# Kernel tuning notes

Measured on AMD Instinct MI355X. Metric: run time of the kernel, lower is better.

Reference implementation:

```python
import jax, jax.numpy as jnp
import numpy as np

N_NODES = 50000
N_EDGES = 800000
IN_DIM = 128
HID = 32
HEADS = 4


def _lin_init(key, fan_in, fan_out):
    k1, k2 = jax.random.split(key)
    s = 1.0 / np.sqrt(fan_in)
    W = jax.random.uniform(k1, (fan_in, fan_out), jnp.float32, -s, s)
    b = jax.random.uniform(k2, (fan_out,), jnp.float32, -s, s)
    return W, b


def setup_inputs() -> dict:
    key = jax.random.key(0)
    keys = jax.random.split(key, 12)
    x = jax.random.normal(keys[0], (N_NODES, IN_DIM), jnp.float32)
    edge_index = jax.random.randint(keys[1], (2, N_EDGES), 0, N_NODES, jnp.int64)

    # conv1: in_dim -> heads*hid (128 -> 4*32)
    Wq1, bq1 = _lin_init(keys[2], IN_DIM, HEADS * HID)
    Wk1, bk1 = _lin_init(keys[3], IN_DIM, HEADS * HID)
    Wv1, bv1 = _lin_init(keys[4], IN_DIM, HEADS * HID)
    Ws1, bs1 = _lin_init(keys[5], IN_DIM, HEADS * HID)
    # conv2: 128 -> 1*32
    Wq2, bq2 = _lin_init(keys[6], HEADS * HID, HID)
    Wk2, bk2 = _lin_init(keys[7], HEADS * HID, HID)
    Wv2, bv2 = _lin_init(keys[8], HEADS * HID, HID)
    Ws2, bs2 = _lin_init(keys[9], HEADS * HID, HID)
    # output linear: 32 -> 1
    Wo, bo = _lin_init(keys[10], HID, 1)

    return {
        "x": x, "edge_index": edge_index,
        "Wq1": Wq1, "bq1": bq1, "Wk1": Wk1, "bk1": bk1,
        "Wv1": Wv1, "bv1": bv1, "Ws1": Ws1, "bs1": bs1,
        "Wq2": Wq2, "bq2": bq2, "Wk2": Wk2, "bk2": bk2,
        "Wv2": Wv2, "bv2": bv2, "Ws2": Ws2, "bs2": bs2,
        "Wo": Wo, "bo": bo,
    }


def transformer_conv(x, edge_index, Wq, bq, Wk, bk, Wv, bv, Ws, bs, heads, d):
    # PyG TransformerConv (concat=True, root_weight=True, beta=False, no edge attr).
    n = x.shape[0]
    src, dst = edge_index[0], edge_index[1]  # message j(src) -> i(dst)
    q = (x @ Wq + bq).reshape(n, heads, d)
    k = (x @ Wk + bk).reshape(n, heads, d)
    v = (x @ Wv + bv).reshape(n, heads, d)
    # per-edge attention logits [E, heads]
    logits = (q[dst] * k[src]).sum(-1) / jnp.sqrt(jnp.float32(d))
    # segment softmax over incoming edges of each target node
    m = jax.ops.segment_max(logits, dst, num_segments=n)
    p = jnp.exp(logits - m[dst])
    denom = jax.ops.segment_sum(p, dst, num_segments=n)
    alpha = p / denom[dst]  # [E, heads]
    # weighted scatter-add of values
    msg = alpha[:, :, None] * v[src]  # [E, heads, d]
    aggr = jax.ops.segment_sum(msg, dst, num_segments=n).reshape(n, heads * d)
    return aggr + x @ Ws + bs  # root (skip) connection


def reference(x, edge_index,
              Wq1, bq1, Wk1, bk1, Wv1, bv1, Ws1, bs1,
              Wq2, bq2, Wk2, bk2, Wv2, bv2, Ws2, bs2,
              Wo, bo):
    h = transformer_conv(x, edge_index, Wq1, bq1, Wk1, bk1, Wv1, bv1, Ws1, bs1, HEADS, HID)
    h = jax.nn.relu(h)
    h = transformer_conv(h, edge_index, Wq2, bq2, Wk2, bk2, Wv2, bv2, Ws2, bs2, 1, HID)
    h = jax.nn.relu(h)
    g = h.mean(axis=0)  # [HID]
    return g @ Wo + bo  # [1]
```

## Files before the change

kernel.cpp:

```cpp
#include <hip/hip_runtime.h>
#include <math.h>

#define N_NODES 50000
#define N_EDGES 800000
#define NBK 196
#define BCAP 6144

typedef short short8 __attribute__((ext_vector_type(8)));
typedef float f32x4 __attribute__((ext_vector_type(4)));
typedef float f32x2 __attribute__((ext_vector_type(2)));

__device__ inline unsigned short f2bf(float v) {
  unsigned u = __float_as_uint(v);
  u += 0x7FFFu + ((u >> 16) & 1u);
  return (unsigned short)(u >> 16);
}
__device__ inline float bf2f(unsigned short b) {
  return __uint_as_float(((unsigned)b) << 16);
}
__device__ inline float bflo(unsigned u) { return __uint_as_float(u << 16); }
__device__ inline float bfhi(unsigned u) { return __uint_as_float(u & 0xFFFF0000u); }
__device__ inline unsigned char f2fp8(float v) {
  return (unsigned char)(__builtin_amdgcn_cvt_pk_fp8_f32(v, 0.f, 0, false) & 0xFF);
}
template <bool HI>
__device__ inline f32x2 fp8dec(unsigned u) {
  return __builtin_amdgcn_cvt_pk_f32_fp8(u, HI);
}

#define SCL 0.17677669529663687f

#define W1_B 256
#define W2_B 64
__global__ void prep_fused(const float* __restrict__ Wq1, const float* __restrict__ Wk1,
                           const float* __restrict__ Wv1, const float* __restrict__ Ws1,
                           const float* __restrict__ bq1, const float* __restrict__ bk1,
                           const float* __restrict__ bv1, const float* __restrict__ bs1,
                           const float* __restrict__ Wq2, const float* __restrict__ Wk2,
                           const float* __restrict__ Wv2, const float* __restrict__ Ws2,
                           const float* __restrict__ bq2, const float* __restrict__ bk2,
                           const float* __restrict__ bv2, const float* __restrict__ bs2,
                           unsigned short* __restrict__ Wt1, float* __restrict__ bcat1,
                           unsigned short* __restrict__ Wt2, float* __restrict__ bcat2,
                           const int* __restrict__ ei, int* __restrict__ bhist, int E) {
  const int b = blockIdx.x, tid = threadIdx.x;
  if (b < W1_B) {
    int i = b * 256 + tid;
    int c = i >> 7, k = i & 127;
    int mi = c >> 7, lc = c & 127;
    const float* W = (mi == 0) ? Wq1 : (mi == 1) ? Wk1 : (mi == 2) ? Wv1 : Ws1;
    float scl = (mi == 0) ? SCL : 1.f;
    Wt1[i] = f2bf(W[(size_t)k * 128 + lc] * scl);
    if (i < 512) {
      int bm = i >> 7, bl = i & 127;
      const float* bb = (bm == 0) ? bq1 : (bm == 1) ? bk1 : (bm == 2) ? bv1 : bs1;
      bcat1[i] = bb[bl] * ((bm == 0) ? SCL : 1.f);
    }
  } else if (b < W1_B + W2_B) {
    int i = (b - W1_B) * 256 + tid;
    int c = i >> 7, k = i & 127;
    int mi = c >> 5, lc = c & 31;
    const float* W = (mi == 0) ? Wq2 : (mi == 1) ? Wk2 : (mi == 2) ? Wv2 : Ws2;
    float scl = (mi == 0) ? SCL : 1.f;
    Wt2[i] = f2bf(W[(size_t)k * 32 + lc] * scl);
    if (i < 128) {
      int bm = i >> 5, bl = i & 31;
      const float* bb = (bm == 0) ? bq2 : (bm == 1) ? bk2 : (bm == 2) ? bv2 : bs2;
      bcat2[i] = bb[bl] * ((bm == 0) ? SCL : 1.f);
    }
  } else {
    __shared__ int h[NBK];
    for (int i = tid; i < NBK; i += 256) h[i] = 0;
    __syncthreads();
    int e = (b - W1_B - W2_B) * 4096 + tid;
#pragma unroll
    for (int p = 0; p < 16; ++p, e += 256)
      if (e < E) atomicAdd(&h[ei[E + e] >> 8], 1);
    __syncthreads();
    for (int i = tid; i < NBK; i += 256)
      if (h[i]) atomicAdd(&bhist[i], h[i]);
  }
}

__global__ void bucket_scan(const int* __restrict__ bhist, int* __restrict__ boff,
                            int* __restrict__ bcur) {
  __shared__ int s[256];
  int t = threadIdx.x;
  int v = (t < NBK) ? bhist[t] : 0;
  s[t] = v;
  __syncthreads();
#pragma unroll
  for (int off = 1; off < 256; off <<= 1) {
    int u = (t >= off) ? s[t - off] : 0;
    __syncthreads();
    s[t] += u;
    __syncthreads();
  }
  if (t < NBK) {
    int excl = s[t] - v;
    boff[t] = excl;
    bcur[t] = excl;
  }
  if (t == NBK - 1) boff[NBK] = s[t];
}

__global__ __launch_bounds__(256) void scatter_gemm1(
    const int* __restrict__ ei, int* __restrict__ bcur, int* __restrict__ ebuck, int E, int EB,
    const float* __restrict__ X, const unsigned short* __restrict__ Wt,
    const float* __restrict__ bcat, unsigned short* __restrict__ Q1b,
    unsigned short* __restrict__ SK1, unsigned char* __restrict__ KV8, int M) {
  __shared__ __align__(16) unsigned char L[3][64 * 272];
  const int tid = threadIdx.x;

  if ((int)blockIdx.x < EB) {
    int* lh = (int*)L[0];
    for (int i = tid; i < NBK; i += 256) lh[i] = 0;
    __syncthreads();
    const int e0 = blockIdx.x * 4096;
    int pks[16], bks[16];
#pragma unroll
    for (int p = 0; p < 16; ++p) {
      int e = e0 + p * 256 + tid;
      if (e < E) {
        int src = ei[e], dst = ei[E + e];
        pks[p] = (src << 8) | (dst & 255);
        bks[p] = dst >> 8;
        atomicAdd(&lh[bks[p]], 1);
      } else bks[p] = -1;
    }
    __syncthreads();
    for (int i = tid; i < NBK; i += 256)
      if (lh[i]) lh[i] = atomicAdd(&bcur[i], lh[i]);
    __syncthreads();
#pragma unroll
    for (int p = 0; p < 16; ++p) {
      if (bks[p] >= 0) {
        int slot = atomicAdd(&lh[bks[p]], 1);
        ebuck[slot] = pks[p];
      }
    }
    return;
  }

  unsigned short* As = (unsigned short*)L[0];
  const int bm = (blockIdx.x - EB) * 64;
  const int wave = tid >> 6, lane = tid & 63;
  const int lr = lane & 15, q = lane >> 4;

#pragma unroll
  for (int p = 0; p < 8; ++p) {
    int f = tid + p * 256;
    int row = f >> 5, c4 = f & 31;
    int gm = bm + row; if (gm >= M) gm = 0;
    float4 v = *(const float4*)(X + (size_t)gm * 128 + c4 * 4);
    ushort4 o;
    o.x = f2bf(v.x); o.y = f2bf(v.y); o.z = f2bf(v.z); o.w = f2bf(v.w);
    *(ushort4*)&As[row * 136 + c4 * 4] = o;
  }
  __syncthreads();

  const int colbase = wave * 128;
  f32x4 acc[4][8];
#pragma unroll
  for (int i = 0; i < 4; ++i)
#pragma unroll
    for (int j = 0; j < 8; ++j) acc[i][j] = (f32x4){0.f, 0.f, 0.f, 0.f};

#pragma unroll
  for (int ks = 0; ks < 4; ++ks) {
    short8 af[4];
#pragma unroll
    for (int i = 0; i < 4; ++i)
      af[i] = *(short8*)&As[(i * 16 + lr) * 136 + ks * 32 + q * 8];
#pragma unroll
    for (int j = 0; j < 8; ++j) {
      short8 bf = *(const short8*)(Wt + (size_t)(colbase + j * 16 + lr) * 128 + ks * 32 + q * 8);
#pragma unroll
      for (int i = 0; i < 4; ++i)
        acc[i][j] = __builtin_amdgcn_mfma_f32_16x16x32_bf16(af[i], bf, acc[i][j], 0, 0, 0);
    }
  }
  __syncthreads();

  float bj[8];
#pragma unroll
  for (int j = 0; j < 8; ++j) bj[j] = bcat[colbase + j * 16 + lr];

  if (wave == 0 || wave == 3) {
    unsigned short* Ls16 = (unsigned short*)((wave == 0) ? L[1] : L[0]);
#pragma unroll
    for (int i = 0; i < 4; ++i)
#pragma unroll
      for (int r = 0; r < 4; ++r) {
        int row = i * 16 + q * 4 + r;
#pragma unroll
        for (int j = 0; j < 8; ++j)
          Ls16[row * 136 + j * 16 + lr] = f2bf(acc[i][j][r] + bj[j]);
      }
  } else {
    unsigned char* KLs = L[2];
    const int voff = (wave == 2) ? 2 : 0;
#pragma unroll
    for (int i = 0; i < 4; ++i)
#pragma unroll
      for (int r = 0; r < 4; ++r) {
        int row = i * 16 + q * 4 + r;
#pragma unroll
        for (int j = 0; j < 8; ++j) {
          int d = j * 16 + lr;
          KLs[row * 272 + 4 * (d >> 1) + voff + (d & 1)] = f2fp8(acc[i][j][r] + bj[j]);
        }
      }
  }
  __syncthreads();

#pragma unroll
  for (int p = 0; p < 4; ++p) {
    int f = tid + p * 256;
    int row = f >> 4, u = f & 15;
    int gr = bm + row;
    if (gr < M) {
      *(uint4*)(Q1b + (size_t)gr * 128 + u * 8) = *(uint4*)&((unsigned short*)L[1])[row * 136 + u * 8];
      *(uint4*)(KV8 + (size_t)gr * 256 + u * 16) = *(uint4*)&L[2][row * 272 + u * 16];
      *(uint4*)(SK1 + (size_t)gr * 128 + u * 8) = *(uint4*)&((unsigned short*)L[0])[row * 136 + u * 8];
    }
  }
}

__global__ void bucket_csr(const int* __restrict__ ebuck, const int* __restrict__ boff,
                           int* __restrict__ rowptr, int* __restrict__ esrc, int N) {
  const int b = blockIdx.x;
  const int lo = boff[b], hi = boff[b + 1];
  const int cnt = hi - lo;
  __shared__ int hist[256];
  __shared__ int cur[256];
  __shared__ int sorted[BCAP];
  const int t = threadIdx.x;
  hist[t] = 0;
  __syncthreads();
  for (int i = t; i < cnt; i += 256) atomicAdd(&hist[ebuck[lo + i] & 255], 1);
  __syncthreads();
  int v = hist[t];
  sorted[t] = v;
  __syncthreads();
#pragma unroll
  for (int off = 1; off < 256; off <<= 1) {
    int u = (t >= off) ? sorted[t - off] : 0;
    __syncthreads();
    sorted[t] += u;
    __syncthreads();
  }
  int excl = sorted[t] - v;
  cur[t] = excl;
  int node = b * 256 + t;
  if (node <= N) rowptr[node] = lo + excl;
  __syncthreads();
  for (int i = t; i < cnt; i += 256) {
    int pk = ebuck[lo + i];
    int slot = atomicAdd(&cur[pk & 255], 1);
    if (slot < BCAP) sorted[slot] = pk;
    else esrc[lo + slot] = pk & 0xFFFFFF00;
  }
  __syncthreads();
  int lim = cnt < BCAP ? cnt : BCAP;
  for (int i = t; i < lim; i += 256) esrc[lo + i] = sorted[i] & 0xFFFFFF00;
}

__global__ __launch_bounds__(256) void gemm2(
    const unsigned short* __restrict__ Ab, const unsigned short* __restrict__ Wt,
    const float* __restrict__ bcat, unsigned char* __restrict__ C2b, int M) {
  __shared__ __align__(16) unsigned short As[64 * 136];
  __shared__ __align__(16) unsigned char Lsb[64 * 272];
  const int bm = blockIdx.x * 64;
  const int tid = threadIdx.x, wave = tid >> 6, lane = tid & 63;
  const int lr = lane & 15, q = lane >> 4;

#pragma unroll
  for (int p = 0; p < 4; ++p) {
    int f = tid + p * 256;
    int row = f >> 4, chunk = f & 15;
    int gm = bm + row; if (gm >= M) gm = 0;
    uint4 v = *(const uint4*)(Ab + (size_t)gm * 128 + chunk * 8);
    *(uint4*)&As[row * 136 + chunk * 8] = v;
  }
  __syncthreads();

  f32x4 acc[4][2];
#pragma unroll
  for (int i = 0; i < 4; ++i)
#pragma unroll
    for (int j = 0; j < 2; ++j) acc[i][j] = (f32x4){0.f, 0.f, 0.f, 0.f};

#pragma unroll
  for (int ks = 0; ks < 4; ++ks) {
    short8 af[4];
#pragma unroll
    for (int i = 0; i < 4; ++i)
      af[i] = *(short8*)&As[(i * 16 + lr) * 136 + ks * 32 + q * 8];
#pragma unroll
    for (int j = 0; j < 2; ++j) {
      short8 bf = *(const short8*)(Wt + (size_t)(wave * 32 + j * 16 + lr) * 128 + ks * 32 + q * 8);
#pragma unroll
      for (int i = 0; i < 4; ++i)
        acc[i][j] = __builtin_amdgcn_mfma_f32_16x16x32_bf16(af[i], bf, acc[i][j], 0, 0, 0);
    }
  }

  float bj[2];
#pragma unroll
  for (int j = 0; j < 2; ++j) bj[j] = bcat[wave * 32 + j * 16 + lr];
#pragma unroll
  for (int i = 0; i < 4; ++i)
#pragma unroll
    for (int r = 0; r < 4; ++r) {
      int row = i * 16 + q * 4 + r;
#pragma unroll
      for (int j = 0; j < 2; ++j) {
        int c = wave * 32 + j * 16 + lr;
        float val = acc[i][j][r] + bj[j];
        if (c < 32) {
          *(unsigned short*)&Lsb[row * 272 + 2 * c] = f2bf(val);
        } else if (c < 64) {
          int d = c - 32;
          Lsb[row * 272 + 64 + 4 * (d >> 1) + (d & 1)] = f2fp8(val);
        } else if (c < 96) {
          int d = c - 64;
          Lsb[row * 272 + 64 + 4 * (d >> 1) + 2 + (d & 1)] = f2fp8(val);
        } else {
          *(unsigned short*)&Lsb[row * 272 + 192 + 2 * (c - 96)] = f2bf(val);
        }
      }
    }
  __syncthreads();
#pragma unroll
  for (int p = 0; p < 16; ++p) {
    int idx = tid + p * 256;
    int row = idx >> 6, u = idx & 63;
    int gr = bm + row;
    if (gr < M) *(unsigned*)(C2b + (size_t)gr * 256 + u * 4) = *(const unsigned*)&Lsb[row * 272 + u * 4];
  }
}

__global__ void node_attn1(const int* __restrict__ rowptr, const int* __restrict__ esrc,
                           const unsigned short* __restrict__ Qb,
                           const unsigned char* __restrict__ KV8,
                           const unsigned short* __restrict__ SK, unsigned short* __restrict__ Hb,
                           int n) {
  int node = (blockIdx.x * blockDim.x + threadIdx.x) >> 6;
  int lane = threadIdx.x & 63;
  if (node >= n) return;
  const int half = lane >> 5, ll = lane & 31;
  const int r0 = rowptr[node], r1 = rowptr[node + 1];
  uint2 qq = *(const uint2*)(Qb + (size_t)node * 128 + ll * 4);
  const float q0 = bflo(qq.x), q1 = bfhi(qq.x), q2 = bflo(qq.y), q3 = bfhi(qq.y);
  float l = 0.f, a0 = 0.f, a1 = 0.f, a2 = 0.f, a3 = 0.f;
  const unsigned char* kvb = KV8 + ll * 8;
  int j = r0;
  for (; j + 8 <= r1; j += 8) {
    int e = j + half * 4;
    int s0 = esrc[e], s1 = esrc[e + 1], s2 = esrc[e + 2], s3 = esrc[e + 3];
    uint2 u0 = *(const uint2*)(kvb + s0);
    uint2 u1 = *(const uint2*)(kvb + s1);
    uint2 u2 = *(const uint2*)(kvb + s2);
    uint2 u3 = *(const uint2*)(kvb + s3);
    f32x2 k0a = fp8dec<false>(u0.x), k0b = fp8dec<false>(u0.y);
    f32x2 k1a = fp8dec<false>(u1.x), k1b = fp8dec<false>(u1.y);
    f32x2 k2a = fp8dec<false>(u2.x), k2b = fp8dec<false>(u2.y);
    f32x2 k3a = fp8dec<false>(u3.x), k3b = fp8dec<false>(u3.y);
    float d0 = q0 * k0a.x + q1 * k0a.y + q2 * k0b.x + q3 * k0b.y;
    float d1 = q0 * k1a.x + q1 * k1a.y + q2 * k1b.x + q3 * k1b.y;
    float d2 = q0 * k2a.x + q1 * k2a.y + q2 * k2b.x + q3 * k2b.y;
    float d3 = q0 * k3a.x + q1 * k3a.y + q2 * k3b.x + q3 * k3b.y;
#pragma unroll
    for (int msk = 1; msk <= 4; msk <<= 1) {
      d0 += __shfl_xor(d0, msk);
      d1 += __shfl_xor(d1, msk);
      d2 += __shfl_xor(d2, msk);
      d3 += __shfl_xor(d3, msk);
    }
    float p0 = __expf(d0), p1 = __expf(d1), p2 = __expf(d2), p3 = __expf(d3);
    l += (p0 + p1) + (p2 + p3);
    f32x2 v0a = fp8dec<true>(u0.x), v0b = fp8dec<true>(u0.y);
    f32x2 v1a = fp8dec<true>(u1.x), v1b = fp8dec<true>(u1.y);
    f32x2 v2a = fp8dec<true>(u2.x), v2b = fp8dec<true>(u2.y);
    f32x2 v3a = fp8dec<true>(u3.x), v3b = fp8dec<true>(u3.y);
    a0 += p0 * v0a.x + p1 * v1a.x + p2 * v2a.x + p3 * v3a.x;
    a1 += p0 * v0a.y + p1 * v1a.y + p2 * v2a.y + p3 * v3a.y;
    a2 += p0 * v0b.x + p1 * v1b.x + p2 * v2b.x + p3 * v3b.x;
    a3 += p0 * v0b.y + p1 * v1b.y + p2 * v2b.y + p3 * v3b.y;
  }
  for (; j < r1; j += 4) {
    int eA = j + half * 2, eB = eA + 1;
    bool vA = eA < r1, vB = eB < r1;
    int sA = esrc[vA ? eA : r0];
    int sB = esrc[vB ? eB : r0];
    uint2 ua = *(const uint2*)(kvb + sA);
    uint2 ub = *(const uint2*)(kvb + sB);
    f32x2 ka1 = fp8dec<false>(ua.x), ka2 = fp8dec<false>(ua.y);
    f32x2 kb1 = fp8dec<false>(ub.x), kb2 = fp8dec<false>(ub.y);
    float dA = q0 * ka1.x + q1 * ka1.y + q2 * ka2.x + q3 * ka2.y;
    float dB = q0 * kb1.x + q1 * kb1.y + q2 * kb2.x + q3 * kb2.y;
#pragma unroll
    for (int msk = 1; msk <= 4; msk <<= 1) {
      dA += __shfl_xor(dA, msk);
      dB += __shfl_xor(dB, msk);
    }
    float pA = vA ? __expf(dA) : 0.f;
    float pB = vB ? __expf(dB) : 0.f;
    l += pA + pB;
    f32x2 va1 = fp8dec<true>(ua.x), va2 = fp8dec<true>(ua.y);
    f32x2 vb1 = fp8dec<true>(ub.x), vb2 = fp8dec<true>(ub.y);
    a0 += pA * va1.x + pB * vb1.x;
    a1 += pA * va1.y + pB * vb1.y;
    a2 += pA * va2.x + pB * vb2.x;
    a3 += pA * va2.y + pB * vb2.y;
  }
  l  += __shfl_xor(l, 32);
  a0 += __shfl_xor(a0, 32);
  a1 += __shfl_xor(a1, 32);
  a2 += __shfl_xor(a2, 32);
  a3 += __shfl_xor(a3, 32);
  float inv = (l > 0.f) ? 1.f / l : 0.f;
  if (half == 0) {
    uint2 sk = *(const uint2*)(SK + (size_t)node * 128 + ll * 4);
    float o0 = fmaxf(bflo(sk.x) + a0 * inv, 0.f);
    float o1 = fmaxf(bfhi(sk.x) + a1 * inv, 0.f);
    float o2 = fmaxf(bflo(sk.y) + a2 * inv, 0.f);
    float o3 = fmaxf(bfhi(sk.y) + a3 * inv, 0.f);
    uint2 hb;
    hb.x = ((unsigned)f2bf(o1) << 16) | (unsigned)f2bf(o0);
    hb.y = ((unsigned)f2bf(o3) << 16) | (unsigned)f2bf(o2);
    *(uint2*)(Hb + (size_t)node * 128 + ll * 4) = hb;
  }
}

__global__ void node_attn2(const int* __restrict__ rowptr, const int* __restrict__ esrc,
                           const unsigned char* __restrict__ C2b, const float* __restrict__ Wo,
                           float* __restrict__ pblock, int n) {
  __shared__ float ps[4];
  int node = (blockIdx.x * blockDim.x + threadIdx.x) >> 6;
  int lane = threadIdx.x & 63;
  int wave = threadIdx.x >> 6;
  const int g = lane >> 4, gl = lane & 15;
  float t = 0.f;
  if (node < n) {
    const int r0 = rowptr[node], r1 = rowptr[node + 1];
    unsigned qu = *(const unsigned*)(C2b + (size_t)node * 256 + gl * 4);
    const float q0 = bflo(qu), q1 = bfhi(qu);
    float l = 0.f, a0 = 0.f, a1 = 0.f;
    const unsigned char* kvb = C2b + 64 + gl * 4;
    int j = r0;
    for (; j + 8 <= r1; j += 8) {
      int e = j + g * 2;
      int s0 = esrc[e], s1 = esrc[e + 1];
      unsigned u0 = *(const unsigned*)(kvb + s0);
      unsigned u1 = *(const unsigned*)(kvb + s1);
      f32x2 k0 = fp8dec<false>(u0), k1 = fp8dec<false>(u1);
      float d0 = q0 * k0.x + q1 * k0.y;
      float d1 = q0 * k1.x + q1 * k1.y;
#pragma unroll
      for (int msk = 1; msk <= 8; msk <<= 1) {
        d0 += __shfl_xor(d0, msk);
        d1 += __shfl_xor(d1, msk);
      }
      float p0 = __expf(d0), p1 = __expf(d1);
      l += p0 + p1;
      f32x2 v0 = fp8dec<true>(u0), v1 = fp8dec<true>(u1);
      a0 += p0 * v0.x + p1 * v1.x;
      a1 += p0 * v0.y + p1 * v1.y;
    }
    for (; j < r1; j += 4) {
      bool v = (j + g) < r1;
      int s = esrc[v ? j + g : r0];
      unsigned u = *(const unsigned*)(kvb + s);
      f32x2 kd = fp8dec<false>(u);
      float d = q0 * kd.x + q1 * kd.y;
#pragma unroll
      for (int msk = 1; msk <= 8; msk <<= 1) d += __shfl_xor(d, msk);
      float p = v ? __expf(d) : 0.f;
      l += p;
      f32x2 vd = fp8dec<true>(u);
      a0 += p * vd.x;
      a1 += p * vd.y;
    }
#pragma unroll
    for (int msk = 16; msk <= 32; msk <<= 1) {
      l  += __shfl_xor(l, msk);
      a0 += __shfl_xor(a0, msk);
      a1 += __shfl_xor(a1, msk);
    }
    float inv = (l > 0.f) ? 1.f / l : 0.f;
    unsigned hu = *(const unsigned*)(C2b + (size_t)node * 256 + 192 + gl * 4);
    float o0 = fmaxf(bflo(hu) + a0 * inv, 0.f);
    float o1 = fmaxf(bfhi(hu) + a1 * inv, 0.f);
    t = o0 * Wo[2 * gl] + o1 * Wo[2 * gl + 1];
#pragma unroll
    for (int msk = 1; msk <= 8; msk <<= 1) t += __shfl_xor(t, msk);
  }
  if (lane == 0) ps[wave] = t;
  __syncthreads();
  if (threadIdx.x == 0) pblock[blockIdx.x] = ps[0] + ps[1] + ps[2] + ps[3];
}

__global__ void final_out(const float* __restrict__ pblock, const float* __restrict__ bo,
                          float* __restrict__ out, int nb, float invN) {
  __shared__ float s[256];
  float acc = 0.f;
  for (int i = threadIdx.x; i < nb; i += 256) acc += pblock[i];
  s[threadIdx.x] = acc;
  __syncthreads();
  for (int off = 128; off >= 1; off >>= 1) {
    if (threadIdx.x < off) s[threadIdx.x] += s[threadIdx.x + off];
    __syncthreads();
  }
  if (threadIdx.x == 0) out[0] = s[0] * invN + bo[0];
}

extern "C" void kernel_launch(void* const* d_in, const int* in_sizes, int n_in,
                              void* d_out, int out_size, void* d_ws, size_t ws_size,
                              hipStream_t stream) {
  const float* x   = (const float*)d_in[0];
  const int*   ei  = (const int*)d_in[1];
  const float* Wq1 = (const float*)d_in[2];  const float* bq1 = (const float*)d_in[3];
  const float* Wk1 = (const float*)d_in[4];  const float* bk1 = (const float*)d_in[5];
  const float* Wv1 = (const float*)d_in[6];  const float* bv1 = (const float*)d_in[7];
  const float* Ws1 = (const float*)d_in[8];  const float* bs1 = (const float*)d_in[9];
  const float* Wq2 = (const float*)d_in[10]; const float* bq2 = (const float*)d_in[11];
  const float* Wk2 = (const float*)d_in[12]; const float* bk2 = (const float*)d_in[13];
  const float* Wv2 = (const float*)d_in[14]; const float* bv2 = (const float*)d_in[15];
  const float* Ws2 = (const float*)d_in[16]; const float* bs2 = (const float*)d_in[17];
  const float* Wo  = (const float*)d_in[18]; const float* bo  = (const float*)d_in[19];

  char* ws = (char*)d_ws;
  const int N = N_NODES, E = N_EDGES;
  const int GB = (N + 63) / 64;
  const int EB = (E + 4095) / 4096;
  const int AB = (N * 64) / 256;

  unsigned short* Q1b = (unsigned short*)(ws + 0);
  unsigned short* SK1 = (unsigned short*)(ws + 12800000);
  unsigned char*  KV1 = (unsigned char*)(ws + 25600000);
  unsigned short* H1b = (unsigned short*)(ws + 51200000);
  unsigned char*  C2  = (unsigned char*)(ws + 64000000);
  int* rowptr = (int*)(ws + 89600000);
  int* esrc   = (int*)(ws + 89900032);
  int* bhist  = (int*)(ws + 93100032);
  int* boff   = (int*)(ws + 93101056);
  int* bcur   = (int*)(ws + 93102080);
  unsigned short* Wt1   = (unsigned short*)(ws + 93103104);
  unsigned short* Wt2   = (unsigned short*)(ws + 93234176);
  float*          bcat1 = (float*)(ws + 93266944);
  float*          bcat2 = (float*)(ws + 93268992);
  float*          pblock = (float*)(ws + 93269504);
  int*            ebuck = (int*)(ws + 93319552);

  float* out = (float*)d_out;

  dim3 blk(256);

  hipMemsetAsync(bhist, 0, NBK * sizeof(int), stream);

  prep_fused<<<dim3(W1_B + W2_B + EB), blk, 0, stream>>>(
      Wq1, Wk1, Wv1, Ws1, bq1, bk1, bv1, bs1,
      Wq2, Wk2, Wv2, Ws2, bq2, bk2, bv2, bs2,
      Wt1, bcat1, Wt2, bcat2, ei, bhist, E);

  bucket_scan<<<dim3(1), blk, 0, stream>>>(bhist, boff, bcur);

  scatter_gemm1<<<dim3(EB + GB), blk, 0, stream>>>(
      ei, bcur, ebuck, E, EB, x, Wt1, bcat1, Q1b, SK1, KV1, N);

  bucket_csr<<<dim3(NBK), blk, 0, stream>>>(ebuck, boff, rowptr, esrc, N);

  node_attn1<<<dim3(AB), blk, 0, stream>>>(rowptr, esrc, Q1b, KV1, SK1, H1b, N);

  gemm2<<<dim3(GB), blk, 0, stream>>>(H1b, Wt2, bcat2, C2, N);

  node_attn2<<<dim3(AB), blk, 0, stream>>>(rowptr, esrc, C2, Wo, pblock, N);

  final_out<<<dim3(1), blk, 0, stream>>>(pblock, bo, out, AB, 1.0f / (float)N);
}
```

Before: 253.3 us.

## Build CSR via per-node degree counting and direct atomic scatter

Replaces the two-level bucket sort with a direct build: prep counts per-node in-degree with global atomics, a new multi-block scan produces rowptr and per-node cursors, and the scatter writes each edge's source straight into its CSR slot via a per-node atomic. This drops the bucket_csr kernel and the intermediate ebuck buffer. It also splits the GEMM1 accumulator into two passes with fewer registers and adds launch_bounds occupancy 4. The trade-off is 800k contended global atomics on per-node counters instead of LDS atomics, plus an extra kernel launch.

After: 290.5 us. 14.7% more time.

```diff
diff --git a/kernel.cpp b/kernel.cpp
--- a/kernel.cpp
+++ b/kernel.cpp
@@ -4,7 +4,6 @@
 #define N_NODES 50000
 #define N_EDGES 800000
 #define NBK 196
-#define BCAP 6144
 
 typedef short short8 __attribute__((ext_vector_type(8)));
 typedef float f32x4 __attribute__((ext_vector_type(4)));
@@ -42,7 +41,8 @@
                            const float* __restrict__ bv2, const float* __restrict__ bs2,
                            unsigned short* __restrict__ Wt1, float* __restrict__ bcat1,
                            unsigned short* __restrict__ Wt2, float* __restrict__ bcat2,
-                           const int* __restrict__ ei, int* __restrict__ bhist, int E) {
+                           const int* __restrict__ ei, int* __restrict__ bhist,
+                           int* __restrict__ deg, int E) {
   const int b = blockIdx.x, tid = threadIdx.x;
   if (b < W1_B) {
     int i = b * 256 + tid;
@@ -75,15 +75,18 @@
     int e = (b - W1_B - W2_B) * 4096 + tid;
 #pragma unroll
     for (int p = 0; p < 16; ++p, e += 256)
-      if (e < E) atomicAdd(&h[ei[E + e] >> 8], 1);
+      if (e < E) {
+        int d = ei[E + e];
+        atomicAdd(&h[d >> 8], 1);
+        atomicAdd(&deg[d], 1);
+      }
     __syncthreads();
     for (int i = tid; i < NBK; i += 256)
       if (h[i]) atomicAdd(&bhist[i], h[i]);
   }
 }
 
-__global__ void bucket_scan(const int* __restrict__ bhist, int* __restrict__ boff,
-                            int* __restrict__ bcur) {
+__global__ void bucket_scan(const int* __restrict__ bhist, int* __restrict__ boff) {
   __shared__ int s[256];
   int t = threadIdx.x;
   int v = (t < NBK) ? bhist[t] : 0;
@@ -96,16 +99,32 @@
     s[t] += u;
     __syncthreads();
   }
-  if (t < NBK) {
-    int excl = s[t] - v;
-    boff[t] = excl;
-    bcur[t] = excl;
-  }
+  if (t < NBK) boff[t] = s[t] - v;
   if (t == NBK - 1) boff[NBK] = s[t];
 }
 
-__global__ __launch_bounds__(256) void scatter_gemm1(
-    const int* __restrict__ ei, int* __restrict__ bcur, int* __restrict__ ebuck, int E, int EB,
+__global__ void rowptr_scan(const int* __restrict__ deg, const int* __restrict__ boff,
+                            int* __restrict__ rowptr, int* __restrict__ nodecur) {
+  __shared__ int s[256];
+  const int b = blockIdx.x, t = threadIdx.x;
+  const int node = b * 256 + t;
+  int v = (node < N_NODES) ? deg[node] : 0;
+  s[t] = v;
+  __syncthreads();
+#pragma unroll
+  for (int off = 1; off < 256; off <<= 1) {
+    int u = (t >= off) ? s[t - off] : 0;
+    __syncthreads();
+    s[t] += u;
+    __syncthreads();
+  }
+  int excl = boff[b] + s[t] - v;
+  if (node <= N_NODES) rowptr[node] = excl;
+  if (node < N_NODES) nodecur[node] = excl;
+}
+
+__global__ __launch_bounds__(256, 4) void scatter_gemm1(
+    const int* __restrict__ ei, int* __restrict__ nodecur, int* __restrict__ esrc, int E, int EB,
     const float* __restrict__ X, const unsigned short* __restrict__ Wt,
     const float* __restrict__ bcat, unsigned short* __restrict__ Q1b,
     unsigned short* __restrict__ SK1, unsigned char* __restrict__ KV8, int M) {
@@ -113,30 +132,21 @@
   const int tid = threadIdx.x;
 
   if ((int)blockIdx.x < EB) {
-    int* lh = (int*)L[0];
-    for (int i = tid; i < NBK; i += 256) lh[i] = 0;
-    __syncthreads();
     const int e0 = blockIdx.x * 4096;
-    int pks[16], bks[16];
+    int srcs[16], dsts[16];
 #pragma unroll
     for (int p = 0; p < 16; ++p) {
       int e = e0 + p * 256 + tid;
       if (e < E) {
-        int src = ei[e], dst = ei[E + e];
-        pks[p] = (src << 8) | (dst & 255);
-        bks[p] = dst >> 8;
-        atomicAdd(&lh[bks[p]], 1);
-      } else bks[p] = -1;
-    }
-    __syncthreads();
-    for (int i = tid; i < NBK; i += 256)
-      if (lh[i]) lh[i] = atomicAdd(&bcur[i], lh[i]);
-    __syncthreads();
+        srcs[p] = ei[e];
+        dsts[p] = ei[E + e];
+      } else dsts[p] = -1;
+    }
 #pragma unroll
     for (int p = 0; p < 16; ++p) {
-      if (bks[p] >= 0) {
-        int slot = atomicAdd(&lh[bks[p]], 1);
-        ebuck[slot] = pks[p];
+      if (dsts[p] >= 0) {
+        int slot = atomicAdd(&nodecur[dsts[p]], 1);
+        esrc[slot] = srcs[p] << 8;
       }
     }
     return;
@@ -159,58 +169,88 @@
   }
   __syncthreads();
 
-  const int colbase = wave * 128;
-  f32x4 acc[4][8];
-#pragma unroll
-  for (int i = 0; i < 4; ++i)
-#pragma unroll
-    for (int j = 0; j < 8; ++j) acc[i][j] = (f32x4){0.f, 0.f, 0.f, 0.f};
-
-#pragma unroll
-  for (int ks = 0; ks < 4; ++ks) {
-    short8 af[4];
+#pragma unroll
+  for (int pass = 0; pass < 2; ++pass) {
+    const int colbase = pass * 256 + wave * 64;
+    f32x4 acc[4][4];
 #pragma unroll
     for (int i = 0; i < 4; ++i)
-      af[i] = *(short8*)&As[(i * 16 + lr) * 136 + ks * 32 + q * 8];
-#pragma unroll
-    for (int j = 0; j < 8; ++j) {
-      short8 bf = *(const short8*)(Wt + (size_t)(colbase + j * 16 + lr) * 128 + ks * 32 + q * 8);
+#pragma unroll
+      for (int j = 0; j < 4; ++j) acc[i][j] = (f32x4){0.f, 0.f, 0.f, 0.f};
+
+#pragma unroll
+    for (int ks = 0; ks < 4; ++ks) {
+      short8 af[4];
 #pragma unroll
       for (int i = 0; i < 4; ++i)
-        acc[i][j] = __builtin_amdgcn_mfma_f32_16x16x32_bf16(af[i], bf, acc[i][j], 0, 0, 0);
-    }
-  }
-  __syncthreads();
-
-  float bj[8];
-#pragma unroll
-  for (int j = 0; j < 8; ++j) bj[j] = bcat[colbase + j * 16 + lr];
-
-  if (wave == 0 || wave == 3) {
-    unsigned short* Ls16 = (unsigned short*)((wave == 0) ? L[1] : L[0]);
-#pragma unroll
-    for (int i = 0; i < 4; ++i)
-#pragma unroll
-      for (int r = 0; r < 4; ++r) {
-        int row = i * 16 + q * 4 + r;
-#pragma unroll
-        for (int j = 0; j < 8; ++j)
-          Ls16[row * 136 + j * 16 + lr] = f2bf(acc[i][j][r] + bj[j]);
-      }
-  } else {
-    unsigned char* KLs = L[2];
-    const int voff = (wave == 2) ? 2 : 0;
-#pragma unroll
-    for (int i = 0; i < 4; ++i)
-#pragma unroll
-      for (int r = 0; r < 4; ++r) {
-        int row = i * 16 + q * 4 + r;
-#pragma unroll
-        for (int j = 0; j < 8; ++j) {
-          int d = j * 16 + lr;
-          KLs[row * 272 + 4 * (d >> 1) + voff + (d & 1)] = f2fp8(acc[i][j][r] + bj[j]);
-        }
-      }
+        af[i] = *(short8*)&As[(i * 16 + lr) * 136 + ks * 32 + q * 8];
+#pragma unroll
+      for (int j = 0; j < 4; ++j) {
+        short8 bf = *(const short8*)(Wt + (size_t)(colbase + j * 16 + lr) * 128 + ks * 32 + q * 8);
+#pragma unroll
+        for (int i = 0; i < 4; ++i)
+          acc[i][j] = __builtin_amdgcn_mfma_f32_16x16x32_bf16(af[i], bf, acc[i][j], 0, 0, 0);
+      }
+    }
+
+    float bj[4];
+#pragma unroll
+    for (int j = 0; j < 4; ++j) bj[j] = bcat[colbase + j * 16 + lr];
+
+    if (pass == 0) {
+      if (wave < 2) {
+        unsigned short* Ls16 = (unsigned short*)L[1];
+#pragma unroll
+        for (int i = 0; i < 4; ++i)
+#pragma unroll
+          for (int r = 0; r < 4; ++r) {
+            int row = i * 16 + q * 4 + r;
+#pragma unroll
+            for (int j = 0; j < 4; ++j)
+              Ls16[row * 136 + wave * 64 + j * 16 + lr] = f2bf(acc[i][j][r] + bj[j]);
+          }
+      } else {
+        unsigned char* KLs = L[2];
+#pragma unroll
+        for (int i = 0; i < 4; ++i)
+#pragma unroll
+          for (int r = 0; r < 4; ++r) {
+            int row = i * 16 + q * 4 + r;
+#pragma unroll
+            for (int j = 0; j < 4; ++j) {
+              int d = (wave - 2) * 64 + j * 16 + lr;
+              KLs[row * 272 + 4 * (d >> 1) + (d & 1)] = f2fp8(acc[i][j][r] + bj[j]);
+            }
+          }
+      }
+    } else {
+      __syncthreads();
+      if (wave < 2) {
+        unsigned char* KLs = L[2];
+#pragma unroll
+        for (int i = 0; i < 4; ++i)
+#pragma unroll
+          for (int r = 0; r < 4; ++r) {
+            int row = i * 16 + q * 4 + r;
+#pragma unroll
+            for (int j = 0; j < 4; ++j) {
+              int d = wave * 64 + j * 16 + lr;
+              KLs[row * 272 + 4 * (d >> 1) + 2 + (d & 1)] = f2fp8(acc[i][j][r] + bj[j]);
+            }
+          }
+      } else {
+        unsigned short* Ls16 = (unsigned short*)L[0];
+#pragma unroll
+        for (int i = 0; i < 4; ++i)
+#pragma unroll
+          for (int r = 0; r < 4; ++r) {
+            int row = i * 16 + q * 4 + r;
+#pragma unroll
+            for (int j = 0; j < 4; ++j)
+              Ls16[row * 136 + (wave - 2) * 64 + j * 16 + lr] = f2bf(acc[i][j][r] + bj[j]);
+          }
+      }
+    }
   }
   __syncthreads();
 
@@ -225,45 +265,6 @@
       *(uint4*)(SK1 + (size_t)gr * 128 + u * 8) = *(uint4*)&((unsigned short*)L[0])[row * 136 + u * 8];
     }
   }
-}
-
-__global__ void bucket_csr(const int* __restrict__ ebuck, const int* __restrict__ boff,
-                           int* __restrict__ rowptr, int* __restrict__ esrc, int N) {
-  const int b = blockIdx.x;
-  const int lo = boff[b], hi = boff[b + 1];
-  const int cnt = hi - lo;
-  __shared__ int hist[256];
-  __shared__ int cur[256];
-  __shared__ int sorted[BCAP];
-  const int t = threadIdx.x;
-  hist[t] = 0;
-  __syncthreads();
-  for (int i = t; i < cnt; i += 256) atomicAdd(&hist[ebuck[lo + i] & 255], 1);
-  __syncthreads();
-  int v = hist[t];
-  sorted[t] = v;
-  __syncthreads();
-#pragma unroll
-  for (int off = 1; off < 256; off <<= 1) {
-    int u = (t >= off) ? sorted[t - off] : 0;
-    __syncthreads();
-    sorted[t] += u;
-    __syncthreads();
-  }
-  int excl = sorted[t] - v;
-  cur[t] = excl;
-  int node = b * 256 + t;
-  if (node <= N) rowptr[node] = lo + excl;
-  __syncthreads();
-  for (int i = t; i < cnt; i += 256) {
-    int pk = ebuck[lo + i];
-    int slot = atomicAdd(&cur[pk & 255], 1);
-    if (slot < BCAP) sorted[slot] = pk;
-    else esrc[lo + slot] = pk & 0xFFFFFF00;
-  }
-  __syncthreads();
-  int lim = cnt < BCAP ? cnt : BCAP;
-  for (int i = t; i < lim; i += 256) esrc[lo + i] = sorted[i] & 0xFFFFFF00;
 }
 
 __global__ __launch_bounds__(256) void gemm2(
@@ -540,37 +541,37 @@
   unsigned short* Q1b = (unsigned short*)(ws + 0);
   unsigned short* SK1 = (unsigned short*)(ws + 12800000);
   unsigned char*  KV1 = (unsigned char*)(ws + 25600000);
-  unsigned short* H1b = (unsigned short*)(ws + 51200000);
-  unsigned char*  C2  = (unsigned char*)(ws + 64000000);
-  int* rowptr = (int*)(ws + 89600000);
-  int* esrc   = (int*)(ws + 89900032);
-  int* bhist  = (int*)(ws + 93100032);
-  int* boff   = (int*)(ws + 93101056);
-  int* bcur   = (int*)(ws + 93102080);
-  unsigned short* Wt1   = (unsigned short*)(ws + 93103104);
-  unsigned short* Wt2   = (unsigned short*)(ws + 93234176);
-  float*          bcat1 = (float*)(ws + 93266944);
-  float*          bcat2 = (float*)(ws + 93268992);
-  float*          pblock = (float*)(ws + 93269504);
-  int*            ebuck = (int*)(ws + 93319552);
+  unsigned short* H1b = (unsigned short*)(ws + 38400000);
+  unsigned char*  C2  = (unsigned char*)(ws + 51200000);
+  int* rowptr  = (int*)(ws + 64000000);
+  int* esrc    = (int*)(ws + 64200704);
+  int* bhist   = (int*)(ws + 67400704);
+  int* deg     = (int*)(ws + 67401728);
+  int* boff    = (int*)(ws + 67602432);
+  int* nodecur = (int*)(ws + 67603456);
+  unsigned short* Wt1   = (unsigned short*)(ws + 67804160);
+  unsigned short* Wt2   = (unsigned short*)(ws + 67935232);
+  float*          bcat1 = (float*)(ws + 67968000);
+  float*          bcat2 = (float*)(ws + 67970048);
+  float*          pblock = (float*)(ws + 67970560);
 
   float* out = (float*)d_out;
 
   dim3 blk(256);
 
-  hipMemsetAsync(bhist, 0, NBK * sizeof(int), stream);
+  hipMemsetAsync(bhist, 0, 201728, stream);
 
   prep_fused<<<dim3(W1_B + W2_B + EB), blk, 0, stream>>>(
       Wq1, Wk1, Wv1, Ws1, bq1, bk1, bv1, bs1,
       Wq2, Wk2, Wv2, Ws2, bq2, bk2, bv2, bs2,
-      Wt1, bcat1, Wt2, bcat2, ei, bhist, E);
-
-  bucket_scan<<<dim3(1), blk, 0, stream>>>(bhist, boff, bcur);
+      Wt1, bcat1, Wt2, bcat2, ei, bhist, deg, E);
+
+  bucket_scan<<<dim3(1), blk, 0, stream>>>(bhist, boff);
+
+  rowptr_scan<<<dim3(NBK), blk, 0, stream>>>(deg, boff, rowptr, nodecur);
 
   scatter_gemm1<<<dim3(EB + GB), blk, 0, stream>>>(
-      ei, bcur, ebuck, E, EB, x, Wt1, bcat1, Q1b, SK1, KV1, N);
-
-  bucket_csr<<<dim3(NBK), blk, 0, stream>>>(ebuck, boff, rowptr, esrc, N);
+      ei, nodecur, esrc, E, EB, x, Wt1, bcat1, Q1b, SK1, KV1, N);
 
   node_attn1<<<dim3(AB), blk, 0, stream>>>(rowptr, esrc, Q1b, KV1, SK1, H1b, N);
 
```
